# Kernel optimization log

Measured on AMD Instinct MI355X. Metric: run time of the kernel, lower is better.

Reference implementation:

```python
import jax, jax.numpy as jnp
import numpy as np

B, N, DIM = 4, 2048, 3
H = 128          # hidden
K = 32           # num_neighbours
L = 4            # num_layers
OUT = 6          # out_per_particle


def _dense_init(key, fan_in, fan_out):
    kw, kb = jax.random.split(key)
    w = jax.random.normal(kw, (fan_in, fan_out), jnp.float32) / np.sqrt(fan_in)
    b = jnp.zeros((fan_out,), jnp.float32)
    return w, b


def setup_inputs() -> dict:
    key = jax.random.key(0)
    ks = jax.random.split(key, 8)
    x = jax.random.normal(ks[0], (B, N, DIM), jnp.float32)
    embed_w, embed_b = _dense_init(ks[1], DIM, H)
    # per-layer stacked params
    miw, mib, mow, mob, uiw, uib, uow, uob = [], [], [], [], [], [], [], []
    for l in range(L):
        k0, k1, k2, k3 = jax.random.split(jax.random.fold_in(ks[2], l), 4)
        w, b = _dense_init(k0, 2 * H + 1, H); miw.append(w); mib.append(b)
        w, b = _dense_init(k1, H, H);         mow.append(w); mob.append(b)
        w, b = _dense_init(k2, 2 * H, H);     uiw.append(w); uib.append(b)
        w, b = _dense_init(k3, H, H);         uow.append(w); uob.append(b)
    out_w, out_b = _dense_init(ks[3], H, OUT)
    return {
        'x': x,
        'embed_w': embed_w, 'embed_b': embed_b,
        'msg_in_w': jnp.stack(miw), 'msg_in_b': jnp.stack(mib),
        'msg_out_w': jnp.stack(mow), 'msg_out_b': jnp.stack(mob),
        'upd_in_w': jnp.stack(uiw), 'upd_in_b': jnp.stack(uib),
        'upd_out_w': jnp.stack(uow), 'upd_out_b': jnp.stack(uob),
        'out_w': out_w, 'out_b': out_b,
    }


def reference(x, embed_w, embed_b,
              msg_in_w, msg_in_b, msg_out_w, msg_out_b,
              upd_in_w, upd_in_b, upd_out_w, upd_out_b,
              out_w, out_b):
    act = jax.nn.silu
    n = x.shape[-2]
    # per-particle embed: (B,N,H)
    h = x @ embed_w + embed_b
    # pairwise squared distances (B,N,N), plain Euclidean (geometry=None)
    diff = x[..., :, None, :] - x[..., None, :, :]
    d_sq = jnp.sum(diff * diff, axis=-1)
    eye = jnp.eye(n, dtype=bool)
    d_sq = jnp.where(eye, jnp.inf, d_sq)
    neg_topk, idx_topk = jax.lax.top_k(-d_sq, K)      # (B,N,K)
    d_nearest = jnp.sqrt(jnp.maximum(-neg_topk, 0.0))  # (B,N,K)

    gather = jax.vmap(lambda hb, ib: hb[ib])  # (N,H),(N,K)->(N,K,H) over batch
    n_layers = msg_in_w.shape[0]
    for l in range(n_layers):
        nb = gather(h, idx_topk)                               # (B,N,K,H)
        node_i = jnp.broadcast_to(h[..., :, None, :], nb.shape)
        msg_inp = jnp.concatenate([node_i, nb, d_nearest[..., None]], axis=-1)
        msg = act(msg_inp @ msg_in_w[l] + msg_in_b[l]) @ msg_out_w[l] + msg_out_b[l]
        agg = jnp.sum(msg, axis=-2)                            # (B,N,H)
        upd_inp = jnp.concatenate([h, agg], axis=-1)
        upd = act(upd_inp @ upd_in_w[l] + upd_in_b[l]) @ upd_out_w[l] + upd_out_b[l]
        h = h + upd
    return h @ out_w + out_b
```

## Files before the change

kernel.cpp:

```cpp
#include <hip/hip_runtime.h>
#include <math.h>

#define B_ 4
#define N_ 2048
#define H_ 128
#define K_ 32
#define L_ 4
#define OUT_ 6
#define BN_ (B_*N_)
#define NPB_E 16
#define NPB_L 16
#define LBLK 512

typedef __attribute__((ext_vector_type(8))) short short8;
typedef __attribute__((ext_vector_type(4))) float f32x4;

#define LDW (H_ + 8)
#define LAYER_W 98304
#define OFF_W1A 0
#define OFF_W1C 16384
#define OFF_W2  32768
#define OFF_U1  49152
#define OFF_U2  81920
#define SCAP 256
#define KNN_ROWS 4
#define KNN_BLKS (BN_/KNN_ROWS)
#define PREP_BLKS (L_*LAYER_W/256)

__device__ __forceinline__ float silu_f(float x) {
    return __fdividef(x, 1.0f + __expf(-x));
}
__device__ __forceinline__ short f2b(float f) {
    unsigned u = __float_as_uint(f);
    return (short)((u + 0x7FFFu + ((u >> 16) & 1u)) >> 16);
}
__device__ __forceinline__ float b2f(short s) {
    return __uint_as_float(((unsigned)(unsigned short)s) << 16);
}
__device__ __forceinline__ unsigned pack2(short lo, short hi) {
    return (unsigned)(unsigned short)lo | ((unsigned)(unsigned short)hi << 16);
}
__device__ __forceinline__ int mbcnt64(unsigned long long m) {
    return __builtin_amdgcn_mbcnt_hi((unsigned)(m >> 32),
           __builtin_amdgcn_mbcnt_lo((unsigned)m, 0));
}

__global__ __launch_bounds__(256) void k_front(
    const float* __restrict__ x, int* __restrict__ nidx, float* __restrict__ ndist,
    const float* __restrict__ miw, const float* __restrict__ mow,
    const float* __restrict__ uiw, const float* __restrict__ uow,
    short* __restrict__ wt)
{
    __shared__ float xsx[N_], xsy[N_], xsz[N_];
    __shared__ unsigned skey[KNN_ROWS][SCAP];
    __shared__ int      sid [KNN_ROWS][SCAP];

    if (blockIdx.x >= KNN_BLKS) {
        int gid = (blockIdx.x - KNN_BLKS) * 256 + threadIdx.x;
        int l = gid / LAYER_W, o = gid - l * LAYER_W;
        float v;
        if (o < OFF_W1C) {
            int n = o >> 7, k = o & 127;
            v = miw[(size_t)l*257*H_ + k*H_ + n];
        } else if (o < OFF_W2) {
            int oo = o - OFF_W1C, n = oo >> 7, k = oo & 127;
            v = miw[(size_t)l*257*H_ + (128 + k)*H_ + n];
        } else if (o < OFF_U1) {
            int oo = o - OFF_W2, n = oo >> 7, k = oo & 127;
            v = mow[(size_t)l*H_*H_ + k*H_ + n];
        } else if (o < OFF_U2) {
            int oo = o - OFF_U1, n = oo >> 8, k = oo & 255;
            v = uiw[(size_t)l*2*H_*H_ + k*H_ + n];
        } else {
            int oo = o - OFF_U2, n = oo >> 7, k = oo & 127;
            v = uow[(size_t)l*H_*H_ + k*H_ + n];
        }
        wt[gid] = f2b(v);
        return;
    }

    int b  = blockIdx.x / (N_/KNN_ROWS);
    int i0 = (blockIdx.x % (N_/KNN_ROWS)) * KNN_ROWS;
    const float* xb = x + (size_t)b*N_*3;
    for (int t = threadIdx.x; t < N_*3; t += 256) {
        float v = xb[t];
        int q = t / 3, r = t - q*3;
        float* dst = (r == 0) ? xsx : (r == 1) ? xsy : xsz;
        dst[q] = v;
    }
    __syncthreads();

    int wave = threadIdx.x >> 6, lane = threadIdx.x & 63;
    int i = i0 + wave;
    float xix = xsx[i], xiy = xsy[i], xiz = xsz[i];

    unsigned u[N_/64];
    unsigned lmin = 0xFFFFFFFFu;
#pragma unroll
    for (int t = 0; t < N_/64; ++t) {
        int j = lane + 64*t;
        float d0 = xix-xsx[j], d1 = xiy-xsy[j], d2 = xiz-xsz[j];
        float d = d0*d0 + d1*d1 + d2*d2;
        unsigned k = (j == i) ? 0x7F800000u : __float_as_uint(d);
        u[t] = k;
        lmin = min(lmin, k);
    }
    unsigned Tup = 0;
#pragma unroll
    for (int bit = 30; bit >= 0; --bit) {
        unsigned cand = Tup | (1u << bit);
        if (__popcll(__ballot(lmin < cand)) < K_) Tup = cand;
    }
    unsigned* sk = skey[wave];
    int*      si = sid [wave];
    int base = 0;
#pragma unroll
    for (int t = 0; t < N_/64; ++t) {
        bool pr = (u[t] <= Tup);
        unsigned long long m = __ballot(pr);
        if (pr) {
            int pos = base + mbcnt64(m);
            if (pos < SCAP) { sk[pos] = u[t]; si[pos] = lane + 64*t; }
        }
        base += __popcll(m);
    }
    int c = min(base, SCAP);
    unsigned sv[4]; int iv[4];
#pragma unroll
    for (int q = 0; q < 4; ++q) {
        int slot = lane + 64*q;
        bool ok = slot < c;
        sv[q] = ok ? sk[slot] : 0xFFFFFFFFu;
        iv[q] = ok ? si[slot] : 0;
    }
    unsigned T = 0;
#pragma unroll
    for (int bit = 30; bit >= 0; --bit) {
        unsigned cand = T | (1u << bit);
        int cnt = __popcll(__ballot(sv[0] < cand)) + __popcll(__ballot(sv[1] < cand))
                + __popcll(__ballot(sv[2] < cand)) + __popcll(__ballot(sv[3] < cand));
        if (cnt < K_) T = cand;
    }
    int cnt_lt = __popcll(__ballot(sv[0] < T)) + __popcll(__ballot(sv[1] < T))
               + __popcll(__ballot(sv[2] < T)) + __popcll(__ballot(sv[3] < T));
    int need = K_ - cnt_lt;
    size_t rbase = ((size_t)(b*N_ + i)) * K_;
    int ltc = 0, eqc = 0;
#pragma unroll
    for (int q = 0; q < 4; ++q) {
        bool lt = sv[q] < T, eq = sv[q] == T;
        unsigned long long mlt = __ballot(lt), meq = __ballot(eq);
        int pp = ltc + mbcnt64(mlt), ee = eqc + mbcnt64(meq);
        ltc += __popcll(mlt); eqc += __popcll(meq);
        int pos = lt ? pp : ((eq && ee < need) ? (cnt_lt + ee) : -1);
        if (pos >= 0) {
            nidx [rbase + pos] = iv[q];
            ndist[rbase + pos] = sqrtf(__uint_as_float(sv[q]));
        }
    }
}

__device__ __forceinline__ void ac_mfma_from_lds(
    const short (*h_l)[LDW], int node0, int tid,
    const short* __restrict__ wt1a, const short* __restrict__ wt1c,
    const float* __restrict__ b1,
    short* __restrict__ a, short* __restrict__ c)
{
    int wave = tid >> 6, lane = tid & 63, l15 = lane & 15, quad = lane >> 4;
    int n = wave*16 + l15;
    f32x4 accA = (f32x4){0.f,0.f,0.f,0.f};
    f32x4 accC = (f32x4){0.f,0.f,0.f,0.f};
#pragma unroll
    for (int kk = 0; kk < 4; ++kk) {
        int k0 = kk*32 + quad*8;
        short8 af = *(const short8*)&h_l[l15][k0];
        short8 bA = *(const short8*)(wt1a + (size_t)n*H_ + k0);
        short8 bC = *(const short8*)(wt1c + (size_t)n*H_ + k0);
        accA = __builtin_amdgcn_mfma_f32_16x16x32_bf16(af, bA, accA, 0, 0, 0);
        accC = __builtin_amdgcn_mfma_f32_16x16x32_bf16(af, bC, accC, 0, 0, 0);
    }
    float b1v = b1[n];
#pragma unroll
    for (int r = 0; r < 4; ++r) {
        int m = quad*4 + r;
        size_t gi = (size_t)(node0+m)*H_ + n;
        a[gi] = f2b(accA[r] + b1v);
        c[gi] = f2b(accC[r]);
    }
}

__global__ __launch_bounds__(LBLK) void k_embed_ac(
    const float* __restrict__ x, const float* __restrict__ ew,
    const float* __restrict__ eb,
    const short* __restrict__ wt1a, const short* __restrict__ wt1c,
    const float* __restrict__ b1,
    float* __restrict__ h, short* __restrict__ a, short* __restrict__ c)
{
    __shared__ __align__(16) short h_l[NPB_E][LDW];
    int blk = blockIdx.x;
    int batch = (blk & 7) >> 1;
    int sub   = ((blk >> 3) << 1) | (blk & 1);
    int node0 = batch * N_ + sub * NPB_E;
    int tid = threadIdx.x;
    for (int t = tid; t < NPB_E*H_; t += LBLK) {
        int row = t >> 7, ch = t & 127;
        int gr = node0 + row;
        float v = eb[ch];
        v = fmaf(x[gr*3+0], ew[ch], v);
        v = fmaf(x[gr*3+1], ew[H_+ch], v);
        v = fmaf(x[gr*3+2], ew[2*H_+ch], v);
        h[(size_t)gr*H_ + ch] = v;
        h_l[row][ch] = f2b(v);
    }
    __syncthreads();
    ac_mfma_from_lds(h_l, node0, tid, wt1a, wt1c, b1, a, c);
}

__global__ __launch_bounds__(LBLK, 4) void k_layer(
    float* __restrict__ h, short* __restrict__ a,
    const int* __restrict__ nidx, const float* __restrict__ ndist,
    const float* __restrict__ wd,
    const short* __restrict__ wl,
    const float* __restrict__ b2, const float* __restrict__ u1b,
    const float* __restrict__ u2b,
    const short* __restrict__ c_rd, short* __restrict__ c_wr,
    const short* __restrict__ wn, const float* __restrict__ b1n, int do_ac,
    const float* __restrict__ ow, const float* __restrict__ ob,
    float* __restrict__ out)
{
    __shared__ __align__(16) short s_l[NPB_L][LDW];
    __shared__ __align__(16) short h_l[NPB_L][LDW];
    __shared__ __align__(16) short agg_l[NPB_L][LDW];
    __shared__ __align__(16) float h32s[NPB_L][H_];
    __shared__ int   idx_s[NPB_L][K_];
    __shared__ float dst_s[NPB_L][K_];
    int blk = blockIdx.x;
    int batch = (blk & 7) >> 1;
    int sub   = ((blk >> 3) << 1) | (blk & 1);
    int node0 = batch * N_ + sub * NPB_L;
    int tid = threadIdx.x;
    int wave = tid >> 6, lane = tid & 63, l15 = lane & 15, quad = lane >> 4;
    int ncol = wave*16 + l15;

    {
        float4 v = reinterpret_cast<const float4*>(h + (size_t)node0*H_)[tid];
        int row = tid >> 5, col = (tid & 31) * 4;
        h_l[row][col+0] = f2b(v.x); h_l[row][col+1] = f2b(v.y);
        h_l[row][col+2] = f2b(v.z); h_l[row][col+3] = f2b(v.w);
        *(float4*)&h32s[row][col] = v;
    }
    idx_s[tid>>5][tid&31] = nidx[(size_t)node0*K_ + tid];
    dst_s[tid>>5][tid&31] = ndist[(size_t)node0*K_ + tid];
    __syncthreads();

    short8 bw2[4], bu1[8], bu2[4];
#pragma unroll
    for (int kk = 0; kk < 4; ++kk)
        bw2[kk] = *(const short8*)(wl + OFF_W2 + (size_t)ncol*H_ + kk*32 + quad*8);
#pragma unroll
    for (int kk = 0; kk < 8; ++kk)
        bu1[kk] = *(const short8*)(wl + OFF_U1 + (size_t)ncol*2*H_ + kk*32 + quad*8);
#pragma unroll
    for (int kk = 0; kk < 4; ++kk)
        bu2[kk] = *(const short8*)(wl + OFF_U2 + (size_t)ncol*H_ + kk*32 + quad*8);

    {
        float wd0 = wd[2*lane], wd1 = wd[2*lane+1];
        const unsigned* c2 = (const unsigned*)c_rd + (size_t)batch*N_*(H_/2);
        const unsigned* a2 = (const unsigned*)a;
#pragma unroll
        for (int nn = 0; nn < 2; ++nn) {
            int m = wave*2 + nn;
            unsigned av = a2[(size_t)(node0+m)*(H_/2) + lane];
            float a0 = b2f((short)(av & 0xFFFFu)), a1 = b2f((short)(av >> 16));
            unsigned cva[16], cvb[16];
#pragma unroll
            for (int k = 0; k < 16; ++k)
                cva[k] = c2[(size_t)idx_s[m][k]*(H_/2) + lane];
#pragma unroll
            for (int k = 0; k < 16; ++k)
                cvb[k] = c2[(size_t)idx_s[m][16+k]*(H_/2) + lane];
            float s0 = 0.f, s1 = 0.f;
#pragma unroll
            for (int k = 0; k < 16; ++k) {
                float dd = dst_s[m][k];
                s0 += silu_f(a0 + fmaf(dd, wd0, b2f((short)(cva[k] & 0xFFFFu))));
                s1 += silu_f(a1 + fmaf(dd, wd1, b2f((short)(cva[k] >> 16))));
            }
#pragma unroll
            for (int k = 0; k < 16; ++k) {
                float dd = dst_s[m][16+k];
                s0 += silu_f(a0 + fmaf(dd, wd0, b2f((short)(cvb[k] & 0xFFFFu))));
                s1 += silu_f(a1 + fmaf(dd, wd1, b2f((short)(cvb[k] >> 16))));
            }
            *(unsigned*)&s_l[m][2*lane] = pack2(f2b(s0), f2b(s1));
        }
    }
    __syncthreads();

    f32x4 acc;
    acc = (f32x4){0,0,0,0};
#pragma unroll
    for (int kk = 0; kk < 4; ++kk) {
        int k0 = kk*32 + quad*8;
        short8 af = *(const short8*)&s_l[l15][k0];
        acc = __builtin_amdgcn_mfma_f32_16x16x32_bf16(af, bw2[kk], acc, 0, 0, 0);
    }
    {
        float b2v = b2[ncol] * (float)K_;
#pragma unroll
        for (int r = 0; r < 4; ++r)
            agg_l[quad*4 + r][ncol] = f2b(acc[r] + b2v);
    }
    __syncthreads();

    acc = (f32x4){0,0,0,0};
#pragma unroll
    for (int kk = 0; kk < 8; ++kk) {
        const short (*src)[LDW] = (kk < 4) ? h_l : agg_l;
        int kloc = ((kk < 4) ? kk*32 : (kk-4)*32) + quad*8;
        short8 af = *(const short8*)&src[l15][kloc];
        acc = __builtin_amdgcn_mfma_f32_16x16x32_bf16(af, bu1[kk], acc, 0, 0, 0);
    }
    short8 bacA[4], bacC[4];
    if (do_ac) {
#pragma unroll
        for (int kk = 0; kk < 4; ++kk) {
            bacA[kk] = *(const short8*)(wn + OFF_W1A + (size_t)ncol*H_ + kk*32 + quad*8);
            bacC[kk] = *(const short8*)(wn + OFF_W1C + (size_t)ncol*H_ + kk*32 + quad*8);
        }
    }
    {
        float u1bv = u1b[ncol];
#pragma unroll
        for (int r = 0; r < 4; ++r)
            s_l[quad*4 + r][ncol] = f2b(silu_f(acc[r] + u1bv));
    }
    __syncthreads();

    acc = (f32x4){0,0,0,0};
#pragma unroll
    for (int kk = 0; kk < 4; ++kk) {
        int k0 = kk*32 + quad*8;
        short8 af = *(const short8*)&s_l[l15][k0];
        acc = __builtin_amdgcn_mfma_f32_16x16x32_bf16(af, bu2[kk], acc, 0, 0, 0);
    }
    {
        float u2bv = u2b[ncol];
#pragma unroll
        for (int r = 0; r < 4; ++r) {
            int m = quad*4 + r;
            float nh = h32s[m][ncol] + acc[r] + u2bv;
            h[(size_t)(node0+m)*H_ + ncol] = nh;
            if (do_ac) h_l[m][ncol] = f2b(nh);
            else       h32s[m][ncol] = nh;
        }
    }
    if (do_ac) {
        __syncthreads();
        int n = ncol;
        f32x4 accA = (f32x4){0,0,0,0}, accC = (f32x4){0,0,0,0};
#pragma unroll
        for (int kk = 0; kk < 4; ++kk) {
            int k0 = kk*32 + quad*8;
            short8 af = *(const short8*)&h_l[l15][k0];
            accA = __builtin_amdgcn_mfma_f32_16x16x32_bf16(af, bacA[kk], accA, 0, 0, 0);
            accC = __builtin_amdgcn_mfma_f32_16x16x32_bf16(af, bacC[kk], accC, 0, 0, 0);
        }
        float b1v = b1n[n];
#pragma unroll
        for (int r = 0; r < 4; ++r) {
            int m = quad*4 + r;
            size_t gi = (size_t)(node0+m)*H_ + n;
            a[gi]    = f2b(accA[r] + b1v);
            c_wr[gi] = f2b(accC[r]);
        }
    } else {
        __syncthreads();
        if (tid < NPB_L*OUT_) {
            int node = tid / OUT_, o = tid - node*OUT_;
            float accv = ob[o];
            for (int r = 0; r < H_; ++r)
                accv = fmaf(h32s[node][r], ow[r*OUT_ + o], accv);
            out[(size_t)(node0+node)*OUT_ + o] = accv;
        }
    }
}

extern "C" void kernel_launch(void* const* d_in, const int* in_sizes, int n_in,
                              void* d_out, int out_size, void* d_ws, size_t ws_size,
                              hipStream_t stream)
{
    const float* x   = (const float*)d_in[0];
    const float* ew  = (const float*)d_in[1];
    const float* eb  = (const float*)d_in[2];
    const float* miw = (const float*)d_in[3];
    const float* mib = (const float*)d_in[4];
    const float* mow = (const float*)d_in[5];
    const float* mob = (const float*)d_in[6];
    const float* uiw = (const float*)d_in[7];
    const float* uib = (const float*)d_in[8];
    const float* uow = (const float*)d_in[9];
    const float* uob = (const float*)d_in[10];
    const float* ow  = (const float*)d_in[11];
    const float* ob  = (const float*)d_in[12];
    float* out = (float*)d_out;

    char* w = (char*)d_ws;
    float* h  = (float*)w;                         w += (size_t)BN_*H_*4;
    float* nd = (float*)w;                         w += (size_t)BN_*K_*4;
    int*   ni = (int*)w;                           w += (size_t)BN_*K_*4;
    short* a  = (short*)w;                         w += (size_t)BN_*H_*2;
    short* c0 = (short*)w;                         w += (size_t)BN_*H_*2;
    short* c1 = (short*)w;                         w += (size_t)BN_*H_*2;
    short* wt = (short*)w;

    k_front<<<KNN_BLKS + PREP_BLKS, 256, 0, stream>>>(x, ni, nd,
        miw, mow, uiw, uow, wt);
    k_embed_ac<<<BN_/NPB_E, LBLK, 0, stream>>>(x, ew, eb,
        wt + OFF_W1A, wt + OFF_W1C, mib, h, a, c0);
    for (int l = 0; l < L_; ++l) {
        const short* c_rd = (l & 1) ? c1 : c0;
        short*       c_wr = (l & 1) ? c0 : c1;
        int do_ac = (l + 1 < L_);
        const short* wn = wt + (size_t)(do_ac ? (l+1) : l) * LAYER_W;
        const float* b1n = mib + (size_t)(do_ac ? (l+1) : l) * H_;
        k_layer<<<BN_/NPB_L, LBLK, 0, stream>>>(h, a, ni, nd,
            miw + (size_t)l*257*H_ + 256*H_,
            wt + (size_t)l*LAYER_W,
            mob + (size_t)l*H_, uib + (size_t)l*H_, uob + (size_t)l*H_,
            c_rd, c_wr, wn, b1n, do_ac,
            ow, ob, out);
    }
}
```

Before: 226.6 us.

## Fold embedding into layer-0 message weights and narrow kNN radix search range

Removes the separate embed+A/C projection kernel. The embed weights are pre-multiplied with the first-layer message weights (Epack, computed by an extra block in k_front), so layer 0 builds the a/c terms straight from 3-D coordinates of the node and its neighbours. This drops one launch and the bf16 a/c round trip through global memory for layer 0, at the cost of per-neighbour 3-FMA recomputation and a different rounding path. Separately, the kNN threshold bisection now starts from the highest differing bit of the wave min/max instead of bit 30, which cuts ballot iterations.

Result: slower. 243.9 us (+7.6%).

```diff
diff --git a/kernel.cpp b/kernel.cpp
--- a/kernel.cpp
+++ b/kernel.cpp
@@ -8,7 +8,6 @@
 #define L_ 4
 #define OUT_ 6
 #define BN_ (B_*N_)
-#define NPB_E 16
 #define NPB_L 16
 #define LBLK 512
 
@@ -49,12 +48,33 @@
     const float* __restrict__ x, int* __restrict__ nidx, float* __restrict__ ndist,
     const float* __restrict__ miw, const float* __restrict__ mow,
     const float* __restrict__ uiw, const float* __restrict__ uow,
-    short* __restrict__ wt)
+    short* __restrict__ wt,
+    const float* __restrict__ ew, const float* __restrict__ eb,
+    const float* __restrict__ mib, float* __restrict__ Epack)
 {
     __shared__ float xsx[N_], xsy[N_], xsz[N_];
     __shared__ unsigned skey[KNN_ROWS][SCAP];
     __shared__ int      sid [KNN_ROWS][SCAP];
 
+    if (blockIdx.x >= KNN_BLKS + PREP_BLKS) {
+        int t = threadIdx.x;
+        int which = t >> 7, n = t & 127;
+        const float* W = miw + (size_t)(which ? 128 : 0) * H_;
+        float E0 = 0.f, E1 = 0.f, E2 = 0.f, Eb = 0.f;
+        for (int k = 0; k < 128; ++k) {
+            float w = W[(size_t)k*H_ + n];
+            E0 = fmaf(ew[k],       w, E0);
+            E1 = fmaf(ew[128 + k], w, E1);
+            E2 = fmaf(ew[256 + k], w, E2);
+            Eb = fmaf(eb[k],       w, Eb);
+        }
+        float* dst = Epack + which * 512;
+        dst[0*128 + n] = E0;
+        dst[1*128 + n] = E1;
+        dst[2*128 + n] = E2;
+        dst[3*128 + n] = Eb + (which ? 0.f : mib[n]);
+        return;
+    }
     if (blockIdx.x >= KNN_BLKS) {
         int gid = (blockIdx.x - KNN_BLKS) * 256 + threadIdx.x;
         int l = gid / LAYER_W, o = gid - l * LAYER_W;
@@ -105,11 +125,19 @@
         u[t] = k;
         lmin = min(lmin, k);
     }
-    unsigned Tup = 0;
-#pragma unroll
-    for (int bit = 30; bit >= 0; --bit) {
-        unsigned cand = Tup | (1u << bit);
-        if (__popcll(__ballot(lmin < cand)) < K_) Tup = cand;
+    unsigned mn = lmin, mx = lmin;
+    for (int off = 32; off; off >>= 1) {
+        unsigned o1 = (unsigned)__shfl_xor((int)mn, off); mn = min(mn, o1);
+        unsigned o2 = (unsigned)__shfl_xor((int)mx, off); mx = max(mx, o2);
+    }
+    unsigned Tup = mn;
+    if (mn != mx) {
+        int hb = 31 - __clz((int)(mn ^ mx));
+        Tup = mn & ~((2u << hb) - 1u);
+        for (int bit = hb; bit >= 0; --bit) {
+            unsigned cand = Tup | (1u << bit);
+            if (__popcll(__ballot(lmin < cand)) < K_) Tup = cand;
+        }
     }
     unsigned* sk = skey[wave];
     int*      si = sid [wave];
@@ -133,13 +161,16 @@
         sv[q] = ok ? sk[slot] : 0xFFFFFFFFu;
         iv[q] = ok ? si[slot] : 0;
     }
-    unsigned T = 0;
-#pragma unroll
-    for (int bit = 30; bit >= 0; --bit) {
-        unsigned cand = T | (1u << bit);
-        int cnt = __popcll(__ballot(sv[0] < cand)) + __popcll(__ballot(sv[1] < cand))
-                + __popcll(__ballot(sv[2] < cand)) + __popcll(__ballot(sv[3] < cand));
-        if (cnt < K_) T = cand;
+    unsigned T = mn;
+    if (mn != Tup) {
+        int hb = 31 - __clz((int)(mn ^ Tup));
+        T = mn & ~((2u << hb) - 1u);
+        for (int bit = hb; bit >= 0; --bit) {
+            unsigned cand = T | (1u << bit);
+            int cnt = __popcll(__ballot(sv[0] < cand)) + __popcll(__ballot(sv[1] < cand))
+                    + __popcll(__ballot(sv[2] < cand)) + __popcll(__ballot(sv[3] < cand));
+            if (cnt < K_) T = cand;
+        }
     }
     int cnt_lt = __popcll(__ballot(sv[0] < T)) + __popcll(__ballot(sv[1] < T))
                + __popcll(__ballot(sv[2] < T)) + __popcll(__ballot(sv[3] < T));
@@ -158,62 +189,6 @@
             ndist[rbase + pos] = sqrtf(__uint_as_float(sv[q]));
         }
     }
-}
-
-__device__ __forceinline__ void ac_mfma_from_lds(
-    const short (*h_l)[LDW], int node0, int tid,
-    const short* __restrict__ wt1a, const short* __restrict__ wt1c,
-    const float* __restrict__ b1,
-    short* __restrict__ a, short* __restrict__ c)
-{
-    int wave = tid >> 6, lane = tid & 63, l15 = lane & 15, quad = lane >> 4;
-    int n = wave*16 + l15;
-    f32x4 accA = (f32x4){0.f,0.f,0.f,0.f};
-    f32x4 accC = (f32x4){0.f,0.f,0.f,0.f};
-#pragma unroll
-    for (int kk = 0; kk < 4; ++kk) {
-        int k0 = kk*32 + quad*8;
-        short8 af = *(const short8*)&h_l[l15][k0];
-        short8 bA = *(const short8*)(wt1a + (size_t)n*H_ + k0);
-        short8 bC = *(const short8*)(wt1c + (size_t)n*H_ + k0);
-        accA = __builtin_amdgcn_mfma_f32_16x16x32_bf16(af, bA, accA, 0, 0, 0);
-        accC = __builtin_amdgcn_mfma_f32_16x16x32_bf16(af, bC, accC, 0, 0, 0);
-    }
-    float b1v = b1[n];
-#pragma unroll
-    for (int r = 0; r < 4; ++r) {
-        int m = quad*4 + r;
-        size_t gi = (size_t)(node0+m)*H_ + n;
-        a[gi] = f2b(accA[r] + b1v);
-        c[gi] = f2b(accC[r]);
-    }
-}
-
-__global__ __launch_bounds__(LBLK) void k_embed_ac(
-    const float* __restrict__ x, const float* __restrict__ ew,
-    const float* __restrict__ eb,
-    const short* __restrict__ wt1a, const short* __restrict__ wt1c,
-    const float* __restrict__ b1,
-    float* __restrict__ h, short* __restrict__ a, short* __restrict__ c)
-{
-    __shared__ __align__(16) short h_l[NPB_E][LDW];
-    int blk = blockIdx.x;
-    int batch = (blk & 7) >> 1;
-    int sub   = ((blk >> 3) << 1) | (blk & 1);
-    int node0 = batch * N_ + sub * NPB_E;
-    int tid = threadIdx.x;
-    for (int t = tid; t < NPB_E*H_; t += LBLK) {
-        int row = t >> 7, ch = t & 127;
-        int gr = node0 + row;
-        float v = eb[ch];
-        v = fmaf(x[gr*3+0], ew[ch], v);
-        v = fmaf(x[gr*3+1], ew[H_+ch], v);
-        v = fmaf(x[gr*3+2], ew[2*H_+ch], v);
-        h[(size_t)gr*H_ + ch] = v;
-        h_l[row][ch] = f2b(v);
-    }
-    __syncthreads();
-    ac_mfma_from_lds(h_l, node0, tid, wt1a, wt1c, b1, a, c);
 }
 
 __global__ __launch_bounds__(LBLK, 4) void k_layer(
@@ -226,12 +201,15 @@
     const short* __restrict__ c_rd, short* __restrict__ c_wr,
     const short* __restrict__ wn, const float* __restrict__ b1n, int do_ac,
     const float* __restrict__ ow, const float* __restrict__ ob,
-    float* __restrict__ out)
+    float* __restrict__ out,
+    const float* __restrict__ x, const float* __restrict__ ew,
+    const float* __restrict__ eb, const float* __restrict__ Epack, int is_l0)
 {
     __shared__ __align__(16) short s_l[NPB_L][LDW];
     __shared__ __align__(16) short h_l[NPB_L][LDW];
     __shared__ __align__(16) short agg_l[NPB_L][LDW];
     __shared__ __align__(16) float h32s[NPB_L][H_];
+    __shared__ float xjs[NPB_L][K_][3];
     __shared__ int   idx_s[NPB_L][K_];
     __shared__ float dst_s[NPB_L][K_];
     int blk = blockIdx.x;
@@ -242,15 +220,34 @@
     int wave = tid >> 6, lane = tid & 63, l15 = lane & 15, quad = lane >> 4;
     int ncol = wave*16 + l15;
 
-    {
+    if (is_l0) {
+        for (int t = tid; t < NPB_L*H_; t += LBLK) {
+            int row = t >> 7, ch = t & 127;
+            int gr = node0 + row;
+            float v = eb[ch];
+            v = fmaf(x[gr*3+0], ew[ch], v);
+            v = fmaf(x[gr*3+1], ew[H_+ch], v);
+            v = fmaf(x[gr*3+2], ew[2*H_+ch], v);
+            h_l[row][ch] = f2b(v);
+            h32s[row][ch] = v;
+        }
+    } else {
         float4 v = reinterpret_cast<const float4*>(h + (size_t)node0*H_)[tid];
         int row = tid >> 5, col = (tid & 31) * 4;
         h_l[row][col+0] = f2b(v.x); h_l[row][col+1] = f2b(v.y);
         h_l[row][col+2] = f2b(v.z); h_l[row][col+3] = f2b(v.w);
         *(float4*)&h32s[row][col] = v;
     }
-    idx_s[tid>>5][tid&31] = nidx[(size_t)node0*K_ + tid];
-    dst_s[tid>>5][tid&31] = ndist[(size_t)node0*K_ + tid];
+    {
+        int j = nidx[(size_t)node0*K_ + tid];
+        int sm = tid >> 5, sk = tid & 31;
+        idx_s[sm][sk] = j;
+        dst_s[sm][sk] = ndist[(size_t)node0*K_ + tid];
+        if (is_l0) {
+            const float* xp = x + ((size_t)batch*N_ + j)*3;
+            xjs[sm][sk][0] = xp[0]; xjs[sm][sk][1] = xp[1]; xjs[sm][sk][2] = xp[2];
+        }
+    }
     __syncthreads();
 
     short8 bw2[4], bu1[8], bu2[4];
@@ -266,34 +263,65 @@
 
     {
         float wd0 = wd[2*lane], wd1 = wd[2*lane+1];
-        const unsigned* c2 = (const unsigned*)c_rd + (size_t)batch*N_*(H_/2);
-        const unsigned* a2 = (const unsigned*)a;
-#pragma unroll
-        for (int nn = 0; nn < 2; ++nn) {
-            int m = wave*2 + nn;
-            unsigned av = a2[(size_t)(node0+m)*(H_/2) + lane];
-            float a0 = b2f((short)(av & 0xFFFFu)), a1 = b2f((short)(av >> 16));
-            unsigned cva[16], cvb[16];
-#pragma unroll
-            for (int k = 0; k < 16; ++k)
-                cva[k] = c2[(size_t)idx_s[m][k]*(H_/2) + lane];
-#pragma unroll
-            for (int k = 0; k < 16; ++k)
-                cvb[k] = c2[(size_t)idx_s[m][16+k]*(H_/2) + lane];
-            float s0 = 0.f, s1 = 0.f;
-#pragma unroll
-            for (int k = 0; k < 16; ++k) {
-                float dd = dst_s[m][k];
-                s0 += silu_f(a0 + fmaf(dd, wd0, b2f((short)(cva[k] & 0xFFFFu))));
-                s1 += silu_f(a1 + fmaf(dd, wd1, b2f((short)(cva[k] >> 16))));
+        int ch0 = 2*lane, ch1 = 2*lane + 1;
+        if (is_l0) {
+            float Ea00 = Epack[ch0],       Ea01 = Epack[ch1];
+            float Ea10 = Epack[128+ch0],   Ea11 = Epack[128+ch1];
+            float Ea20 = Epack[256+ch0],   Ea21 = Epack[256+ch1];
+            float ea0  = Epack[384+ch0],   ea1  = Epack[384+ch1];
+            float Ec00 = Epack[512+ch0],   Ec01 = Epack[512+ch1];
+            float Ec10 = Epack[640+ch0],   Ec11 = Epack[640+ch1];
+            float Ec20 = Epack[768+ch0],   Ec21 = Epack[768+ch1];
+            float ec0  = Epack[896+ch0],   ec1  = Epack[896+ch1];
+#pragma unroll
+            for (int nn = 0; nn < 2; ++nn) {
+                int m = wave*2 + nn;
+                int gr = node0 + m;
+                float xi0 = x[gr*3], xi1 = x[gr*3+1], xi2 = x[gr*3+2];
+                float a0 = fmaf(xi2, Ea20, fmaf(xi1, Ea10, fmaf(xi0, Ea00, ea0)));
+                float a1 = fmaf(xi2, Ea21, fmaf(xi1, Ea11, fmaf(xi0, Ea01, ea1)));
+                float s0 = 0.f, s1 = 0.f;
+#pragma unroll
+                for (int k = 0; k < K_; ++k) {
+                    float xj0 = xjs[m][k][0], xj1 = xjs[m][k][1], xj2 = xjs[m][k][2];
+                    float dd = dst_s[m][k];
+                    float c0 = fmaf(xj2, Ec20, fmaf(xj1, Ec10, fmaf(xj0, Ec00, ec0)));
+                    float c1 = fmaf(xj2, Ec21, fmaf(xj1, Ec11, fmaf(xj0, Ec01, ec1)));
+                    s0 += silu_f(a0 + fmaf(dd, wd0, c0));
+                    s1 += silu_f(a1 + fmaf(dd, wd1, c1));
+                }
+                *(unsigned*)&s_l[m][2*lane] = pack2(f2b(s0), f2b(s1));
             }
-#pragma unroll
-            for (int k = 0; k < 16; ++k) {
-                float dd = dst_s[m][16+k];
-                s0 += silu_f(a0 + fmaf(dd, wd0, b2f((short)(cvb[k] & 0xFFFFu))));
-                s1 += silu_f(a1 + fmaf(dd, wd1, b2f((short)(cvb[k] >> 16))));
+        } else {
+            const unsigned* c2 = (const unsigned*)c_rd + (size_t)batch*N_*(H_/2);
+            const unsigned* a2 = (const unsigned*)a;
+#pragma unroll
+            for (int nn = 0; nn < 2; ++nn) {
+                int m = wave*2 + nn;
+                unsigned av = a2[(size_t)(node0+m)*(H_/2) + lane];
+                float a0 = b2f((short)(av & 0xFFFFu)), a1 = b2f((short)(av >> 16));
+                unsigned cva[16], cvb[16];
+#pragma unroll
+                for (int k = 0; k < 16; ++k)
+                    cva[k] = c2[(size_t)idx_s[m][k]*(H_/2) + lane];
+#pragma unroll
+                for (int k = 0; k < 16; ++k)
+                    cvb[k] = c2[(size_t)idx_s[m][16+k]*(H_/2) + lane];
+                float s0 = 0.f, s1 = 0.f;
+#pragma unroll
+                for (int k = 0; k < 16; ++k) {
+                    float dd = dst_s[m][k];
+                    s0 += silu_f(a0 + fmaf(dd, wd0, b2f((short)(cva[k] & 0xFFFFu))));
+                    s1 += silu_f(a1 + fmaf(dd, wd1, b2f((short)(cva[k] >> 16))));
+                }
+#pragma unroll
+                for (int k = 0; k < 16; ++k) {
+                    float dd = dst_s[m][16+k];
+                    s0 += silu_f(a0 + fmaf(dd, wd0, b2f((short)(cvb[k] & 0xFFFFu))));
+                    s1 += silu_f(a1 + fmaf(dd, wd1, b2f((short)(cvb[k] >> 16))));
+                }
+                *(unsigned*)&s_l[m][2*lane] = pack2(f2b(s0), f2b(s1));
             }
-            *(unsigned*)&s_l[m][2*lane] = pack2(f2b(s0), f2b(s1));
         }
     }
     __syncthreads();
@@ -413,12 +441,11 @@
     short* a  = (short*)w;                         w += (size_t)BN_*H_*2;
     short* c0 = (short*)w;                         w += (size_t)BN_*H_*2;
     short* c1 = (short*)w;                         w += (size_t)BN_*H_*2;
-    short* wt = (short*)w;
-
-    k_front<<<KNN_BLKS + PREP_BLKS, 256, 0, stream>>>(x, ni, nd,
-        miw, mow, uiw, uow, wt);
-    k_embed_ac<<<BN_/NPB_E, LBLK, 0, stream>>>(x, ew, eb,
-        wt + OFF_W1A, wt + OFF_W1C, mib, h, a, c0);
+    short* wt = (short*)w;                         w += (size_t)L_*LAYER_W*2;
+    float* Epack = (float*)w;
+
+    k_front<<<KNN_BLKS + PREP_BLKS + 1, 256, 0, stream>>>(x, ni, nd,
+        miw, mow, uiw, uow, wt, ew, eb, mib, Epack);
     for (int l = 0; l < L_; ++l) {
         const short* c_rd = (l & 1) ? c1 : c0;
         short*       c_wr = (l & 1) ? c0 : c1;
@@ -430,6 +457,7 @@
             wt + (size_t)l*LAYER_W,
             mob + (size_t)l*H_, uib + (size_t)l*H_, uob + (size_t)l*H_,
             c_rd, c_wr, wn, b1n, do_ac,
-            ow, ob, out);
-    }
-}
+            ow, ob, out,
+            x, ew, eb, Epack, (l == 0) ? 1 : 0);
+    }
+}
```
